# Performance work log

Hardware: AMD Instinct MI355X
Metric: run time of the kernel (lower is better)

Reference implementation:

```python
import jax, jax.numpy as jnp
import numpy as np

N, C_IN, C_OUT, H, W = 16, 256, 256, 32, 32
K = 9  # 3x3 kernel


def setup_inputs() -> dict:
    key = jax.random.key(0)
    k1, k2, k3 = jax.random.split(key, 3)
    x = jax.random.normal(k1, (N, C_IN, H, W), dtype=jnp.float32)
    # offsets as produced upstream from anchors: (N, H*W, 18)
    offset = jax.random.normal(k2, (N, H * W, 2 * K), dtype=jnp.float32)
    # DeformConv weight (no bias), kaiming-ish scale
    weight = jax.random.normal(k3, (C_OUT, C_IN, 3, 3), dtype=jnp.float32) * 0.02
    return {"x": x, "offset": offset, "weight": weight}


def _deform_conv3x3(x, offset_nchw, weight):
    """DeformConv v1, kernel 3x3, stride 1, padding 1, dilation 1,
    groups=1, deformable_groups=1, zero padding outside borders."""
    n, c, h, w = x.shape
    o = weight.shape[0]
    # offset channel layout: (dy_k, dx_k) pairs for k = 0..8
    off = offset_nchw.reshape(n, K, 2, h, w)
    dy = off[:, :, 0]  # (N,K,H,W)
    dx = off[:, :, 1]
    ky = (jnp.arange(K) // 3 - 1).astype(x.dtype)  # kernel row offsets -1,0,1
    kx = (jnp.arange(K) % 3 - 1).astype(x.dtype)
    base_y = jnp.arange(h, dtype=x.dtype)[None, None, :, None]
    base_x = jnp.arange(w, dtype=x.dtype)[None, None, None, :]
    py = base_y + ky[None, :, None, None] + dy  # (N,K,H,W) sample rows
    px = base_x + kx[None, :, None, None] + dx  # (N,K,H,W) sample cols

    y0 = jnp.floor(py)
    x0 = jnp.floor(px)
    ly = py - y0  # fractional parts
    lx = px - x0

    x_flat = x.reshape(n, c, h * w)

    def corner(yi, xi, wgt):
        valid = (yi >= 0) & (yi <= h - 1) & (xi >= 0) & (xi <= w - 1)
        yc = jnp.clip(yi, 0, h - 1).astype(jnp.int32)
        xc = jnp.clip(xi, 0, w - 1).astype(jnp.int32)
        idx = (yc * w + xc).reshape(n, K * h * w)
        g = jax.vmap(lambda xf, i: xf[:, i])(x_flat, idx)  # (N,C,K*H*W)
        wv = (wgt * valid.astype(x.dtype)).reshape(n, 1, K * h * w)
        return g * wv

    val = (corner(y0, x0, (1 - ly) * (1 - lx))
           + corner(y0, x0 + 1, (1 - ly) * lx)
           + corner(y0 + 1, x0, ly * (1 - lx))
           + corner(y0 + 1, x0 + 1, ly * lx))
    val = val.reshape(n, c, K, h, w)  # sampled im2col columns
    return jnp.einsum('nckhw,ock->nohw', val, weight.reshape(o, c, K))


def reference(x, offset, weight):
    n, _, h, w = x.shape
    assert h * w == offset.shape[1]
    # AdaptiveConv.forward: (N, HW, 18) -> (N, 18, H, W)
    offset_nchw = jnp.transpose(offset, (0, 2, 1)).reshape(n, 2 * K, h, w)
    return _deform_conv3x3(x, offset_nchw, weight)
```

## Files before the change

kernel.cpp:

```cpp
#include <hip/hip_runtime.h>

#define NB   16
#define CIN  256
#define COUT 256
#define HH   32
#define WW   32
#define HW   1024
#define KK   9
#define CK   2304

typedef __bf16 bf16x8 __attribute__((ext_vector_type(8)));
typedef float  f32x4  __attribute__((ext_vector_type(4)));

__device__ __forceinline__ unsigned short f2bf(float f) {
    unsigned int u = __float_as_uint(f);
    u += 0x7FFFu + ((u >> 16) & 1u);
    return (unsigned short)(u >> 16);
}
__device__ __forceinline__ float bfhi(unsigned int u) {
    return __uint_as_float(u & 0xFFFF0000u);
}
__device__ __forceinline__ float bflo(unsigned int u) {
    return __uint_as_float(u << 16);
}
__device__ __forceinline__ unsigned pk2(float lo, float hi) {
    unsigned r;
    asm("v_cvt_pk_bf16_f32 %0, %1, %2" : "=v"(r) : "v"(lo), "v"(hi));
    return r;
}

typedef const __attribute__((address_space(1))) void* gas_ptr;
typedef __attribute__((address_space(3))) void* las_ptr;

__device__ __forceinline__ void async16(const void* g, void* l) {
    __builtin_amdgcn_global_load_lds((gas_ptr)g, (las_ptr)l, 16, 0, 0);
}

#define SB() __builtin_amdgcn_sched_barrier(0)
#define SYNC() do { SB(); asm volatile("s_waitcnt lgkmcnt(0)" ::: "memory"); SB(); \
                    __builtin_amdgcn_s_barrier(); SB(); } while (0)

__global__ __launch_bounds__(256) void prep_kernel(const float* __restrict__ w,
                                                   unsigned short* __restrict__ wbf,
                                                   const float* __restrict__ x,
                                                   unsigned short* __restrict__ xtb) {
    __shared__ float lsbuf[64 * 65];
    const int t = threadIdx.x;

    if (blockIdx.x < 256) {
        const int o = blockIdx.x;
        const float* wo = w + (size_t)o * CK;
#pragma unroll
        for (int i = t; i < CK; i += 256) lsbuf[i] = wo[i];
        __syncthreads();
        unsigned short* dst = wbf + (size_t)o * CK;
#pragma unroll
        for (int i = t; i < CK; i += 256) {
            int k = i >> 8, c = i & 255;
            dst[i] = f2bf(lsbuf[c * KK + k]);
        }
        return;
    }

    float (*ls)[65] = (float(*)[65])lsbuf;
    const int id  = blockIdx.x - 256;
    const int c0  = (id & 3) << 6;
    const int hw0 = ((id >> 2) & 15) << 6;
    const int n   = id >> 6;
    {
        int c = t >> 2, q = t & 3;
        const float4* base = (const float4*)(x + ((size_t)(n * CIN + c0 + c)) * HW + hw0 + q * 16);
#pragma unroll
        for (int j = 0; j < 4; ++j) {
            float4 v = base[j];
            ls[c][q * 16 + j * 4 + 0] = v.x;
            ls[c][q * 16 + j * 4 + 1] = v.y;
            ls[c][q * 16 + j * 4 + 2] = v.z;
            ls[c][q * 16 + j * 4 + 3] = v.w;
        }
    }
    __syncthreads();
    {
        int hw = t >> 2, seg = (t & 3) * 16;
        unsigned int dw[8];
#pragma unroll
        for (int j = 0; j < 8; ++j) {
            float f0 = ls[seg + 2 * j][hw];
            float f1 = ls[seg + 2 * j + 1][hw];
            dw[j] = (unsigned)f2bf(f0) | ((unsigned)f2bf(f1) << 16);
        }
        uint4* dst = (uint4*)(xtb + ((size_t)(n * HW + hw0 + hw)) * CIN + c0 + seg);
        dst[0] = *(uint4*)&dw[0];
        dst[1] = *(uint4*)&dw[4];
    }
}

__global__ __launch_bounds__(512, 2) void fused_kernel(const unsigned short* __restrict__ wbf,
                                                       const unsigned short* __restrict__ xtb,
                                                       const float* __restrict__ off,
                                                       float* __restrict__ out) {
    __shared__ unsigned short As[3][256 * 64];
    __shared__ unsigned short Bs[2][64 * 64];

    const int tid  = threadIdx.x;
    const int wv   = tid >> 6;
    const int lane = tid & 63;
    const int quad = lane >> 4;
    const int l15  = lane & 15;

    const int hw_local = tid >> 3;
    const int seg      = tid & 7;

    const int id  = blockIdx.x;
    const int n   = ((id & 7) << 1) | ((id >> 3) & 1);
    const int hw0 = (id >> 4) * 64;

    const int hw = hw0 + hw_local;
    const int h  = hw >> 5, w = hw & 31;

    const int srow   = lane >> 3;
    const int schunk = (lane & 7) ^ (srow & 7);

    const uint4*  xb4  = (const uint4*)(xtb + (size_t)n * HW * CIN);
    const float2* offp = (const float2*)(off + ((size_t)n * HW + hw) * (2 * KK));

    f32x4 acc[2][4] = {};

    auto setup2 = [&](float2 o, int tapv, float* wg, int* ix) {
        float py = (float)(h + tapv / 3 - 1) + o.x;
        float px = (float)(w + tapv % 3 - 1) + o.y;
        float y0f = floorf(py), x0f = floorf(px);
        float ly = py - y0f, lx = px - x0f;
        int y0 = (int)y0f, x0 = (int)x0f;
#pragma unroll
        for (int c2 = 0; c2 < 4; ++c2) {
            int yy = y0 + (c2 >> 1);
            int xx = x0 + (c2 & 1);
            float wy = (c2 >> 1) ? ly : 1.0f - ly;
            float wx = (c2 & 1) ? lx : 1.0f - lx;
            bool v = (yy >= 0) && (yy < HH) && (xx >= 0) && (xx < WW);
            wg[c2] = v ? wy * wx : 0.0f;
            int yc = yy < 0 ? 0 : (yy > HH - 1 ? HH - 1 : yy);
            int xc = xx < 0 ? 0 : (xx > WW - 1 ? WW - 1 : xx);
            ix[c2] = yc * WW + xc;
        }
    };

    auto loadc = [&](uint4 cr[4], const int* ix, int q) {
#pragma unroll
        for (int c2 = 0; c2 < 4; ++c2)
            cr[c2] = xb4[(size_t)ix[c2] * 32 + q * 8 + seg];
    };

    auto dmaA = [&](int ai, int kblk) {
        const unsigned short* wsrc = wbf + (size_t)kblk * 64 + (size_t)srow * CK + schunk * 8;
        unsigned short* dst = &As[ai][0];
#pragma unroll
        for (int j = 0; j < 4; ++j) {
            int rb = wv * 32 + j * 8;
            async16(wsrc + (size_t)rb * CK, dst + rb * 64);
        }
    };

    auto lerpB = [&](int bi, const uint4 cr[4], const float* wg) {
        unsigned u0[4], u1[4], u2[4], u3[4];
        *(uint4*)u0 = cr[0]; *(uint4*)u1 = cr[1];
        *(uint4*)u2 = cr[2]; *(uint4*)u3 = cr[3];
        unsigned dw[4];
#pragma unroll
        for (int d = 0; d < 4; ++d) {
            float lo = wg[0] * bflo(u0[d]) + wg[1] * bflo(u1[d])
                     + wg[2] * bflo(u2[d]) + wg[3] * bflo(u3[d]);
            float hi = wg[0] * bfhi(u0[d]) + wg[1] * bfhi(u1[d])
                     + wg[2] * bfhi(u2[d]) + wg[3] * bfhi(u3[d]);
            dw[d] = pk2(lo, hi);
        }
        *(uint4*)&Bs[bi][hw_local * 64 + (seg ^ (hw_local & 7)) * 8] = *(uint4*)dw;
    };

    auto frag_read = [&](int ai, int bi, bf16x8 af[2][2], bf16x8 bfr[4][2]) {
        const unsigned short* Ap = &As[ai][0];
        const unsigned short* Bp = &Bs[bi][0];
#pragma unroll
        for (int mi = 0; mi < 2; ++mi)
#pragma unroll
            for (int hh = 0; hh < 2; ++hh) {
                int row = wv * 32 + mi * 16 + l15;
                int ch  = (hh * 4 + quad) ^ (row & 7);
                af[mi][hh] = *(const bf16x8*)(Ap + row * 64 + ch * 8);
            }
#pragma unroll
        for (int ni = 0; ni < 4; ++ni)
#pragma unroll
            for (int hh = 0; hh < 2; ++hh) {
                int row = ni * 16 + l15;
                int ch  = (hh * 4 + quad) ^ (row & 7);
                bfr[ni][hh] = *(const bf16x8*)(Bp + row * 64 + ch * 8);
            }
    };

    auto frag_mma = [&](bf16x8 af[2][2], bf16x8 bfr[4][2]) {
        __builtin_amdgcn_s_setprio(1);
#pragma unroll
        for (int mi = 0; mi < 2; ++mi)
#pragma unroll
            for (int ni = 0; ni < 4; ++ni) {
                acc[mi][ni] = __builtin_amdgcn_mfma_f32_16x16x32_bf16(af[mi][0], bfr[ni][0], acc[mi][ni], 0, 0, 0);
                acc[mi][ni] = __builtin_amdgcn_mfma_f32_16x16x32_bf16(af[mi][1], bfr[ni][1], acc[mi][ni], 0, 0, 0);
            }
        __builtin_amdgcn_s_setprio(0);
    };

    float wgc[4], wgn[4];
    int   ixc[4], ixn[4];
    uint4 crA[4], crB[4];
    {
        float2 o0 = offp[0];
        setup2(o0, 0, wgc, ixc);
        dmaA(0, 0);
        dmaA(1, 1);
        SB();
        loadc(crA, ixc, 0);
        loadc(crB, ixc, 1);
        SB();
        lerpB(0, crA, wgc);
        SYNC();
    }

    int i0 = 0;
#pragma unroll 1
    for (int tap = 0; tap < 9; ++tap) {
        const int i1 = (i0 == 2) ? 0 : i0 + 1;
        const int i2 = (i1 == 2) ? 0 : i1 + 1;
        const int kb = tap * 4;
        const bool more = (tap < 8);
        bf16x8 af[2][2], bfr[4][2];
        float2 onx = {};

        frag_read(i0, 0, af, bfr);
        SB();
        dmaA(i2, kb + 2);
        SB();
        lerpB(1, crB, wgc);
        SB();
        loadc(crA, ixc, 2);
        SB();
        frag_mma(af, bfr);
        SYNC();

        frag_read(i1, 1, af, bfr);
        SB();
        dmaA(i0, kb + 3);
        SB();
        lerpB(0, crA, wgc);
        SB();
        loadc(crB, ixc, 3);
        if (more) onx = offp[tap + 1];
        SB();
        frag_mma(af, bfr);
        SYNC();

        frag_read(i2, 0, af, bfr);
        SB();
        if (more) dmaA(i1, kb + 4);
        SB();
        lerpB(1, crB, wgc);
        SB();
        if (more) { setup2(onx, tap + 1, wgn, ixn); loadc(crA, ixn, 0); }
        SB();
        frag_mma(af, bfr);
        SYNC();

        frag_read(i0, 1, af, bfr);
        SB();
        if (more) {
            dmaA(i2, kb + 5);
            SB();
            lerpB(0, crA, wgn);
            SB();
            loadc(crB, ixn, 1);
#pragma unroll
            for (int c2 = 0; c2 < 4; ++c2) { wgc[c2] = wgn[c2]; ixc[c2] = ixn[c2]; }
            SB();
            frag_mma(af, bfr);
            SYNC();
        } else {
            frag_mma(af, bfr);
        }
        i0 = i1;
    }

    float* opnt = out + (size_t)n * COUT * HW + hw0;
#pragma unroll
    for (int mi = 0; mi < 2; ++mi)
#pragma unroll
        for (int ni = 0; ni < 4; ++ni) {
            int col = ni * 16 + l15;
#pragma unroll
            for (int rr = 0; rr < 4; ++rr) {
                int row = wv * 32 + mi * 16 + quad * 4 + rr;
                opnt[(size_t)row * HW + col] = acc[mi][ni][rr];
            }
        }
}

extern "C" void kernel_launch(void* const* d_in, const int* in_sizes, int n_in,
                              void* d_out, int out_size, void* d_ws, size_t ws_size,
                              hipStream_t stream) {
    const float* x   = (const float*)d_in[0];
    const float* off = (const float*)d_in[1];
    const float* wt  = (const float*)d_in[2];
    float* out = (float*)d_out;

    unsigned short* wbf = (unsigned short*)d_ws;
    unsigned short* xtb = (unsigned short*)((char*)d_ws + 1179648);

    prep_kernel<<<1280, 256, 0, stream>>>(wt, wbf, x, xtb);
    fused_kernel<<<256, 512, 0, stream>>>(wbf, xtb, off, out);
}
```

Baseline: 110.7 us.

## Split fused kernel into consumer MFMA waves and producer gather/DMA waves

Adds four producer wavefronts per block (768 threads) that handle weight DMA, bilinear gathers and lerp into shared memory. The original eight waves now only read fragments and issue MFMAs, so the sampling work is specialised away from the matrix math. Producers each handle two pixel rows and eight weight rows, which doubles their per-thread register load and gather count. Launch bounds change to (768,3), which may constrain registers and occupancy.

```diff
diff --git a/kernel.cpp b/kernel.cpp
--- a/kernel.cpp
+++ b/kernel.cpp
@@ -95,7 +95,7 @@
     }
 }
 
-__global__ __launch_bounds__(512, 2) void fused_kernel(const unsigned short* __restrict__ wbf,
+__global__ __launch_bounds__(768, 3) void fused_kernel(const unsigned short* __restrict__ wbf,
                                                        const unsigned short* __restrict__ xtb,
                                                        const float* __restrict__ off,
                                                        float* __restrict__ out) {
@@ -105,30 +105,34 @@
     const int tid  = threadIdx.x;
     const int wv   = tid >> 6;
     const int lane = tid & 63;
-    const int quad = lane >> 4;
-    const int l15  = lane & 15;
-
-    const int hw_local = tid >> 3;
-    const int seg      = tid & 7;
+    const bool cons = (wv < 8);
 
     const int id  = blockIdx.x;
     const int n   = ((id & 7) << 1) | ((id >> 3) & 1);
     const int hw0 = (id >> 4) * 64;
 
-    const int hw = hw0 + hw_local;
-    const int h  = hw >> 5, w = hw & 31;
-
+    const int quad = lane >> 4;
+    const int l15  = lane & 15;
+
+    const int ptid = tid - 512;
+    const int pwv  = wv - 8;
+    const int hwA  = (ptid >> 3) & 31;
+    const int seg  = ptid & 7;
     const int srow   = lane >> 3;
     const int schunk = (lane & 7) ^ (srow & 7);
 
-    const uint4*  xb4  = (const uint4*)(xtb + (size_t)n * HW * CIN);
-    const float2* offp = (const float2*)(off + ((size_t)n * HW + hw) * (2 * KK));
+    const int hA = (hw0 + hwA) >> 5,      wA = (hw0 + hwA) & 31;
+    const int hB = (hw0 + hwA + 32) >> 5, wB = (hw0 + hwA + 32) & 31;
+
+    const uint4*  xb4   = (const uint4*)(xtb + (size_t)n * HW * CIN);
+    const float2* offpA = (const float2*)(off + ((size_t)n * HW + hw0 + hwA) * (2 * KK));
+    const float2* offpB = offpA + 32 * KK;
 
     f32x4 acc[2][4] = {};
 
-    auto setup2 = [&](float2 o, int tapv, float* wg, int* ix) {
-        float py = (float)(h + tapv / 3 - 1) + o.x;
-        float px = (float)(w + tapv % 3 - 1) + o.y;
+    auto setup2 = [&](float2 o, int tapv, int hh_, int ww_, float* wg, int* ix) {
+        float py = (float)(hh_ + tapv / 3 - 1) + o.x;
+        float px = (float)(ww_ + tapv % 3 - 1) + o.y;
         float y0f = floorf(py), x0f = floorf(px);
         float ly = py - y0f, lx = px - x0f;
         int y0 = (int)y0f, x0 = (int)x0f;
@@ -146,36 +150,43 @@
         }
     };
 
-    auto loadc = [&](uint4 cr[4], const int* ix, int q) {
-#pragma unroll
-        for (int c2 = 0; c2 < 4; ++c2)
-            cr[c2] = xb4[(size_t)ix[c2] * 32 + q * 8 + seg];
-    };
-
-    auto dmaA = [&](int ai, int kblk) {
+    auto loadcP = [&](uint4 cr[2][4], const int* ixA, const int* ixB, int q) {
+#pragma unroll
+        for (int c2 = 0; c2 < 4; ++c2) {
+            cr[0][c2] = xb4[(size_t)ixA[c2] * 32 + q * 8 + seg];
+            cr[1][c2] = xb4[(size_t)ixB[c2] * 32 + q * 8 + seg];
+        }
+    };
+
+    auto dmaP = [&](int ai, int kblk) {
         const unsigned short* wsrc = wbf + (size_t)kblk * 64 + (size_t)srow * CK + schunk * 8;
         unsigned short* dst = &As[ai][0];
 #pragma unroll
-        for (int j = 0; j < 4; ++j) {
-            int rb = wv * 32 + j * 8;
+        for (int j = 0; j < 8; ++j) {
+            int rb = pwv * 64 + j * 8;
             async16(wsrc + (size_t)rb * CK, dst + rb * 64);
         }
     };
 
-    auto lerpB = [&](int bi, const uint4 cr[4], const float* wg) {
-        unsigned u0[4], u1[4], u2[4], u3[4];
-        *(uint4*)u0 = cr[0]; *(uint4*)u1 = cr[1];
-        *(uint4*)u2 = cr[2]; *(uint4*)u3 = cr[3];
-        unsigned dw[4];
-#pragma unroll
-        for (int d = 0; d < 4; ++d) {
-            float lo = wg[0] * bflo(u0[d]) + wg[1] * bflo(u1[d])
-                     + wg[2] * bflo(u2[d]) + wg[3] * bflo(u3[d]);
-            float hi = wg[0] * bfhi(u0[d]) + wg[1] * bfhi(u1[d])
-                     + wg[2] * bfhi(u2[d]) + wg[3] * bfhi(u3[d]);
-            dw[d] = pk2(lo, hi);
-        }
-        *(uint4*)&Bs[bi][hw_local * 64 + (seg ^ (hw_local & 7)) * 8] = *(uint4*)dw;
+    auto lerpP = [&](int bi, const uint4 cr[2][4], const float* wgA2, const float* wgB2) {
+#pragma unroll
+        for (int p = 0; p < 2; ++p) {
+            const float* wg = p ? wgB2 : wgA2;
+            int row = hwA + p * 32;
+            unsigned u0[4], u1[4], u2[4], u3[4];
+            *(uint4*)u0 = cr[p][0]; *(uint4*)u1 = cr[p][1];
+            *(uint4*)u2 = cr[p][2]; *(uint4*)u3 = cr[p][3];
+            unsigned dw[4];
+#pragma unroll
+            for (int d = 0; d < 4; ++d) {
+                float lo = wg[0] * bflo(u0[d]) + wg[1] * bflo(u1[d])
+                         + wg[2] * bflo(u2[d]) + wg[3] * bflo(u3[d]);
+                float hi = wg[0] * bfhi(u0[d]) + wg[1] * bfhi(u1[d])
+                         + wg[2] * bfhi(u2[d]) + wg[3] * bfhi(u3[d]);
+                dw[d] = pk2(lo, hi);
+            }
+            *(uint4*)&Bs[bi][row * 64 + (seg ^ (row & 7)) * 8] = *(uint4*)dw;
+        }
     };
 
     auto frag_read = [&](int ai, int bi, bf16x8 af[2][2], bf16x8 bfr[4][2]) {
@@ -211,21 +222,24 @@
         __builtin_amdgcn_s_setprio(0);
     };
 
-    float wgc[4], wgn[4];
-    int   ixc[4], ixn[4];
-    uint4 crA[4], crB[4];
-    {
-        float2 o0 = offp[0];
-        setup2(o0, 0, wgc, ixc);
-        dmaA(0, 0);
-        dmaA(1, 1);
+    float wgcA[4], wgcB[4], wgnA[4], wgnB[4];
+    int   ixcA[4], ixcB[4], ixnA[4], ixnB[4];
+    uint4 crA[2][4], crB[2][4];
+    float2 onxA = {}, onxB = {};
+
+    if (!cons) {
+        float2 oA = offpA[0], oB = offpB[0];
+        setup2(oA, 0, hA, wA, wgcA, ixcA);
+        setup2(oB, 0, hB, wB, wgcB, ixcB);
+        dmaP(0, 0);
+        dmaP(1, 1);
         SB();
-        loadc(crA, ixc, 0);
-        loadc(crB, ixc, 1);
+        loadcP(crA, ixcA, ixcB, 0);
+        loadcP(crB, ixcA, ixcB, 1);
         SB();
-        lerpB(0, crA, wgc);
-        SYNC();
-    }
+        lerpP(0, crA, wgcA, wgcB);
+    }
+    SYNC();
 
     int i0 = 0;
 #pragma unroll 1
@@ -235,73 +249,85 @@
         const int kb = tap * 4;
         const bool more = (tap < 8);
         bf16x8 af[2][2], bfr[4][2];
-        float2 onx = {};
-
-        frag_read(i0, 0, af, bfr);
-        SB();
-        dmaA(i2, kb + 2);
-        SB();
-        lerpB(1, crB, wgc);
-        SB();
-        loadc(crA, ixc, 2);
-        SB();
-        frag_mma(af, bfr);
+
+        if (cons) {
+            frag_read(i0, 0, af, bfr);
+            SB();
+            frag_mma(af, bfr);
+        } else {
+            dmaP(i2, kb + 2);
+            SB();
+            lerpP(1, crB, wgcA, wgcB);
+            SB();
+            loadcP(crA, ixcA, ixcB, 2);
+        }
         SYNC();
 
-        frag_read(i1, 1, af, bfr);
-        SB();
-        dmaA(i0, kb + 3);
-        SB();
-        lerpB(0, crA, wgc);
-        SB();
-        loadc(crB, ixc, 3);
-        if (more) onx = offp[tap + 1];
-        SB();
-        frag_mma(af, bfr);
+        if (cons) {
+            frag_read(i1, 1, af, bfr);
+            SB();
+            frag_mma(af, bfr);
+        } else {
+            dmaP(i0, kb + 3);
+            SB();
+            lerpP(0, crA, wgcA, wgcB);
+            SB();
+            loadcP(crB, ixcA, ixcB, 3);
+            if (more) { onxA = offpA[tap + 1]; onxB = offpB[tap + 1]; }
+        }
         SYNC();
 
-        frag_read(i2, 0, af, bfr);
-        SB();
-        if (more) dmaA(i1, kb + 4);
-        SB();
-        lerpB(1, crB, wgc);
-        SB();
-        if (more) { setup2(onx, tap + 1, wgn, ixn); loadc(crA, ixn, 0); }
-        SB();
-        frag_mma(af, bfr);
+        if (cons) {
+            frag_read(i2, 0, af, bfr);
+            SB();
+            frag_mma(af, bfr);
+        } else {
+            if (more) dmaP(i1, kb + 4);
+            SB();
+            lerpP(1, crB, wgcA, wgcB);
+            SB();
+            if (more) {
+                setup2(onxA, tap + 1, hA, wA, wgnA, ixnA);
+                setup2(onxB, tap + 1, hB, wB, wgnB, ixnB);
+                loadcP(crA, ixnA, ixnB, 0);
+            }
+        }
         SYNC();
 
-        frag_read(i0, 1, af, bfr);
-        SB();
-        if (more) {
-            dmaA(i2, kb + 5);
-            SB();
-            lerpB(0, crA, wgn);
-            SB();
-            loadc(crB, ixn, 1);
-#pragma unroll
-            for (int c2 = 0; c2 < 4; ++c2) { wgc[c2] = wgn[c2]; ixc[c2] = ixn[c2]; }
+        if (cons) {
+            frag_read(i0, 1, af, bfr);
             SB();
             frag_mma(af, bfr);
-            SYNC();
-        } else {
-            frag_mma(af, bfr);
-        }
+        } else if (more) {
+            dmaP(i2, kb + 5);
+            SB();
+            lerpP(0, crA, wgnA, wgnB);
+            SB();
+            loadcP(crB, ixnA, ixnB, 1);
+#pragma unroll
+            for (int c2 = 0; c2 < 4; ++c2) {
+                wgcA[c2] = wgnA[c2]; wgcB[c2] = wgnB[c2];
+                ixcA[c2] = ixnA[c2]; ixcB[c2] = ixnB[c2];
+            }
+        }
+        if (more) SYNC();
         i0 = i1;
     }
 
-    float* opnt = out + (size_t)n * COUT * HW + hw0;
-#pragma unroll
-    for (int mi = 0; mi < 2; ++mi)
-#pragma unroll
-        for (int ni = 0; ni < 4; ++ni) {
-            int col = ni * 16 + l15;
-#pragma unroll
-            for (int rr = 0; rr < 4; ++rr) {
-                int row = wv * 32 + mi * 16 + quad * 4 + rr;
-                opnt[(size_t)row * HW + col] = acc[mi][ni][rr];
-            }
-        }
+    if (cons) {
+        float* opnt = out + (size_t)n * COUT * HW + hw0;
+#pragma unroll
+        for (int mi = 0; mi < 2; ++mi)
+#pragma unroll
+            for (int ni = 0; ni < 4; ++ni) {
+                int col = ni * 16 + l15;
+#pragma unroll
+                for (int rr = 0; rr < 4; ++rr) {
+                    int row = wv * 32 + mi * 16 + quad * 4 + rr;
+                    opnt[(size_t)row * HW + col] = acc[mi][ni][rr];
+                }
+            }
+    }
 }
 
 extern "C" void kernel_launch(void* const* d_in, const int* in_sizes, int n_in,
@@ -316,5 +342,5 @@
     unsigned short* xtb = (unsigned short*)((char*)d_ws + 1179648);
 
     prep_kernel<<<1280, 256, 0, stream>>>(wt, wbf, x, xtb);
-    fused_kernel<<<256, 512, 0, stream>>>(wbf, xtb, off, out);
-}
+    fused_kernel<<<256, 768, 0, stream>>>(wbf, xtb, off, out);
+}
```

Measured after the change: 305.3 us. 2.76x slower.
